# Performance work log

Measured on AMD Instinct MI355X. Metric: run time of the kernel, lower is better.

The kernel has to match this reference:

```python
import jax, jax.numpy as jnp
import numpy as np
from jax import lax

# ---- Haar (db1) wavelet filters, matching create_wavelet_filter ----
_S2 = float(1.0 / np.sqrt(2.0))
_dec_lo = np.array([_S2, _S2], np.float32)    # pywt dec_lo reversed (symmetric)
_dec_hi = np.array([_S2, -_S2], np.float32)   # pywt dec_hi [-s,s] reversed
_rec_lo = np.array([_S2, _S2], np.float32)    # pywt rec_lo flipped (symmetric)
_rec_hi = np.array([-_S2, _S2], np.float32)   # pywt rec_hi [s,-s] flipped

def _outer(a, b):  # torch: a.unsqueeze(0) * b.unsqueeze(1) -> [i,j] = a[j]*b[i]
    return b[:, None] * a[None, :]

DEC = jnp.asarray(np.stack([_outer(_dec_lo, _dec_lo), _outer(_dec_lo, _dec_hi),
                            _outer(_dec_hi, _dec_lo), _outer(_dec_hi, _dec_hi)]))  # [4,2,2]
REC = jnp.asarray(np.stack([_outer(_rec_lo, _rec_lo), _outer(_rec_lo, _rec_hi),
                            _outer(_rec_hi, _rec_lo), _outer(_rec_hi, _rec_hi)]))  # [4,2,2]

BN_EPS = 1e-5

def mish(x):
    return x * jnp.tanh(jax.nn.softplus(x))

def silu(x):
    return x * jax.nn.sigmoid(x)

def bn(x, g, b):  # eval-mode BatchNorm2d with running_mean=0, running_var=1
    return x * (g / jnp.sqrt(1.0 + BN_EPS))[None, :, None, None] + b[None, :, None, None]

def dwconv(x, w, pad):  # depthwise conv, w: [C,1,k,k]
    return lax.conv_general_dilated(x, w, (1, 1), [(pad, pad), (pad, pad)],
                                    feature_group_count=x.shape[1],
                                    dimension_numbers=('NCHW', 'OIHW', 'NCHW'))

def dyn_dwconv(x, ew, gw):
    # DynamicConv2d (depthwise experts). ew: [E,C,1,k,k], gw: [E,C]
    gates = jax.nn.softmax(x.mean((2, 3)) @ gw.T, axis=-1)  # [B,E]
    k = ew.shape[-1]
    outs = jnp.stack([dwconv(x, ew[e], k // 2) for e in range(ew.shape[0])], 1)  # [B,E,C,H,W]
    return jnp.einsum('be,bechw->bchw', gates, outs)

def local_branch(x, ew, gw, bn1g, bn1b, pw, bn2g, bn2b):
    # DWConv2d_BN_ReLU: dynamic dwconv -> BN -> Mish -> depthwise 1x1 (per-channel scale) -> BN
    y = mish(bn(dyn_dwconv(x, ew, gw), bn1g, bn1b))
    y = y * pw[None, :, None, None]
    return bn(y, bn2g, bn2b)

def sel_scan(u, xw, dtw, dtb, Alog, Dp):
    # u: [B,L,D]; xw: [R+2N,D]; dtw: [D,R]; dtb: [D]; Alog: [D,N]; Dp: [D]
    R = dtw.shape[1]
    N = Alog.shape[1]
    xdbl = jnp.einsum('bld,ed->ble', u, xw)
    dt, Bm, Cm = xdbl[..., :R], xdbl[..., R:R + N], xdbl[..., R + N:]
    delta = jax.nn.softplus(jnp.einsum('blr,dr->bld', dt, dtw) + dtb)  # [B,L,D]
    A = -jnp.exp(Alog)                                                  # [D,N]
    a = jnp.exp(delta[..., None] * A)                                   # [B,L,D,N]
    b = delta[..., None] * Bm[:, :, None, :] * u[..., None]             # [B,L,D,N]
    def comb(c1, c2):
        a1, b1 = c1
        a2, b2 = c2
        return a1 * a2, a2 * b1 + b2
    _, h = lax.associative_scan(comb, (a, b), axis=1)                    # h_t = a_t h_{t-1} + b_t
    return jnp.einsum('bldn,bln->bld', h, Cm) + Dp * u

def ss2d(x, in_w, cw, cb, xpw, dtw, dtb, Alog, Dp, ow):
    # SS2D (d_state=1, k_group=2, channel_first): in_proj -> dwconv+silu -> 2-direction
    # selective scan -> gate with silu(z) -> out_proj.
    B, C, H, W = x.shape
    xz = jnp.einsum('oc,bchw->bohw', in_w, x)
    d = in_w.shape[0] // 2
    xi, z = xz[:, :d], xz[:, d:]
    xc = silu(dwconv(xi, cw, 1) + cb[None, :, None, None])
    u0 = xc.reshape(B, d, H * W).transpose(0, 2, 1)                       # row-major scan
    u1 = xc.transpose(0, 1, 3, 2).reshape(B, d, H * W).transpose(0, 2, 1)  # col-major scan
    y0 = sel_scan(u0, xpw[0], dtw[0], dtb[0], Alog[0], Dp[0])
    y1 = sel_scan(u1, xpw[1], dtw[1], dtb[1], Alog[1], Dp[1])
    y0 = y0.transpose(0, 2, 1).reshape(B, d, H, W)
    y1 = y1.transpose(0, 2, 1).reshape(B, d, W, H).transpose(0, 1, 3, 2)
    y = (y0 + y1) * silu(z)
    return jnp.einsum('oc,bchw->bohw', ow, y)

def mbwt(x, wav_w, wav_b, wav_scale, base_scale,
         ss_in_w, ss_conv_w, ss_conv_b, ss_xproj_w, ss_dt_w, ss_dt_b, ss_A_log, ss_D, ss_out_w):
    # MBWTConv2d, wt_levels=1, H/W even. Haar WT (2x2 stride 2) == block reshape + einsum.
    B, C, H, W = x.shape
    xr = x.reshape(B, C, H // 2, 2, W // 2, 2)
    wt = jnp.einsum('bchpwq,kpq->bckhw', xr, DEC)                  # [B,C,4,h,w]
    tag = wt.reshape(B, 4 * C, H // 2, W // 2)
    tag = dwconv(tag, wav_w, wav_w.shape[-1] // 2) + wav_b[None, :, None, None]
    tag = (tag * wav_scale).reshape(B, C, 4, H // 2, W // 2)
    # inverse Haar WT (conv_transpose 2x2 stride 2, groups=C)
    up = jnp.einsum('bckhw,kpq->bchpwq', tag, REC).reshape(B, C, H, W)
    g = ss2d(x, ss_in_w, ss_conv_w, ss_conv_b, ss_xproj_w, ss_dt_w, ss_dt_b, ss_A_log, ss_D, ss_out_w)
    return base_scale * g + up


def setup_inputs() -> dict:
    key = jax.random.key(0)
    ks = iter(jax.random.split(key, 64))
    B, DIM, H, W = 16, 256, 64, 64
    Cg = Cl = 64
    d = {'x': jax.random.normal(next(ks), (B, DIM, H, W), jnp.float32)}
    for j, k in enumerate((3, 5, 7)):
        p = f'l{j}_'
        d[p + 'ew'] = jax.random.normal(next(ks), (4, Cl, 1, k, k), jnp.float32) * 0.1
        d[p + 'gw'] = jax.random.normal(next(ks), (4, Cl), jnp.float32) * 0.1
        d[p + 'bn1g'] = jnp.ones((Cl,), jnp.float32)
        d[p + 'bn1b'] = jnp.zeros((Cl,), jnp.float32)
        d[p + 'pw'] = jax.random.normal(next(ks), (Cl,), jnp.float32) * 0.2
        d[p + 'bn2g'] = jnp.ones((Cl,), jnp.float32)
        d[p + 'bn2b'] = jnp.zeros((Cl,), jnp.float32)
    d['wav_w'] = jax.random.normal(next(ks), (4 * Cg, 1, 3, 3), jnp.float32) * 0.1
    d['wav_b'] = jnp.zeros((4 * Cg,), jnp.float32)
    d['wav_scale'] = jnp.full((1, 4 * Cg, 1, 1), 0.1, jnp.float32)
    d['base_scale'] = jnp.ones((1, Cg, 1, 1), jnp.float32)
    dm, R, N, K = Cg, 4, 1, 2  # d_inner, dt_rank, d_state, k_group
    d['ss_in_w'] = jax.random.normal(next(ks), (2 * dm, Cg), jnp.float32) * float(1 / np.sqrt(Cg))
    d['ss_conv_w'] = jax.random.normal(next(ks), (dm, 1, 3, 3), jnp.float32) * 0.1
    d['ss_conv_b'] = jnp.zeros((dm,), jnp.float32)
    d['ss_xproj_w'] = jax.random.normal(next(ks), (K, R + 2 * N, dm), jnp.float32) * float(1 / np.sqrt(dm))
    d['ss_dt_w'] = jax.random.normal(next(ks), (K, dm, R), jnp.float32) * float(1 / np.sqrt(R))
    d['ss_dt_b'] = jnp.full((K, dm), -2.0, jnp.float32)
    d['ss_A_log'] = jnp.zeros((K, dm, N), jnp.float32)
    d['ss_D'] = jnp.ones((K, dm), jnp.float32)
    d['ss_out_w'] = jax.random.normal(next(ks), (Cg, dm), jnp.float32) * float(1 / np.sqrt(dm))
    return d


def reference(x,
              l0_ew, l0_gw, l0_bn1g, l0_bn1b, l0_pw, l0_bn2g, l0_bn2b,
              l1_ew, l1_gw, l1_bn1g, l1_bn1b, l1_pw, l1_bn2g, l1_bn2b,
              l2_ew, l2_gw, l2_bn1g, l2_bn1b, l2_pw, l2_bn2g, l2_bn2b,
              wav_w, wav_b, wav_scale, base_scale,
              ss_in_w, ss_conv_w, ss_conv_b, ss_xproj_w, ss_dt_w, ss_dt_b, ss_A_log, ss_D, ss_out_w):
    Cg, Cl = 64, 64
    xg, xl, xi = x[:, :Cg], x[:, Cg:Cg + Cl], x[:, Cg + Cl:]
    yl = (local_branch(xl, l0_ew, l0_gw, l0_bn1g, l0_bn1b, l0_pw, l0_bn2g, l0_bn2b)
          + local_branch(xl, l1_ew, l1_gw, l1_bn1g, l1_bn1b, l1_pw, l1_bn2g, l1_bn2b)
          + local_branch(xl, l2_ew, l2_gw, l2_bn1g, l2_bn1b, l2_pw, l2_bn2g, l2_bn2b))
    yg = mbwt(xg, wav_w, wav_b, wav_scale, base_scale,
              ss_in_w, ss_conv_w, ss_conv_b, ss_xproj_w, ss_dt_w, ss_dt_b, ss_A_log, ss_D, ss_out_w)
    return jnp.concatenate([yg, yl, xi], axis=1)
```

## Files before the change

kernel.cpp:

```cpp
#include <hip/hip_runtime.h>
#include <math.h>

static constexpr int NB   = 16;
static constexpr int DIM  = 256;
static constexpr int CG   = 64;
static constexpr int HH   = 64;
static constexpr int WW   = 64;
static constexpr int HW   = HH * WW;

__device__ __forceinline__ float mish_fast(float x) {
    float t = __expf(fminf(x, 20.f));
    float p = __builtin_fmaf(t, t, t + t);
    return x * p * __builtin_amdgcn_rcpf(p + 2.f);
}
__device__ __forceinline__ float silu_f(float x) {
    return x * __builtin_amdgcn_rcpf(1.f + __expf(-x));
}
__device__ __forceinline__ float softplus_fast(float x) {
    return fmaxf(x, 0.f) + __logf(1.f + __expf(-fabsf(x)));
}

__global__ __launch_bounds__(256) void k_stage1(
    const float* __restrict__ x,
    const float* __restrict__ wav_w, const float* __restrict__ wav_b,
    const float* __restrict__ wav_scale,
    float* __restrict__ up, float* __restrict__ mean,
    const float* __restrict__ in_w,
    float* __restrict__ xi, float* __restrict__ z) {
    __shared__ float smem[8192];
    int bid = blockIdx.x;
    int tid = threadIdx.x;

    if (bid % 3 != 2) {
        int aid = (bid / 3) * 2 + (bid % 3);
        int c = aid & 63, b = aid >> 6;
        float* wtb = smem;
        float* red = smem + 4352;
        const float* xp = x + ((size_t)b * DIM + c) * HW;

        {
            const float4* lp4 = (const float4*)(x + ((size_t)b * DIM + 64 + c) * HW);
            float s = 0.f;
            for (int i = tid; i < 1024; i += 256) {
                float4 v = lp4[i];
                s += (v.x + v.y) + (v.z + v.w);
            }
            red[tid] = s;
            __syncthreads();
            for (int o = 128; o > 0; o >>= 1) {
                if (tid < o) red[tid] += red[tid + o];
                __syncthreads();
            }
            if (tid == 0) mean[b * 64 + c] = red[0] * (1.f / HW);
        }

#pragma unroll
        for (int it = 0; it < 2; ++it) {
            int p = tid + it * 256;
            int h = p >> 4, w2 = p & 15;
            float4 top = *(const float4*)(xp + (2 * h) * 64 + 4 * w2);
            float4 bot = *(const float4*)(xp + (2 * h + 1) * 64 + 4 * w2);
            float a0 = top.x, b0 = top.y, c0q = bot.x, d0 = bot.y;
            float a1 = top.z, b1 = top.w, c1q = bot.z, d1 = bot.w;
            int base0 = h * 34 + 2 * w2;
            *(float2*)(wtb + 0 * 1088 + base0) =
                make_float2(0.5f * (a0 + b0 + c0q + d0), 0.5f * (a1 + b1 + c1q + d1));
            *(float2*)(wtb + 1 * 1088 + base0) =
                make_float2(0.5f * (a0 + b0 - c0q - d0), 0.5f * (a1 + b1 - c1q - d1));
            *(float2*)(wtb + 2 * 1088 + base0) =
                make_float2(0.5f * (a0 - b0 + c0q - d0), 0.5f * (a1 - b1 + c1q - d1));
            *(float2*)(wtb + 3 * 1088 + base0) =
                make_float2(0.5f * (a0 - b0 - c0q + d0), 0.5f * (a1 - b1 - c1q + d1));
        }
        __syncthreads();

        float wk[4][9], tb[4];
#pragma unroll
        for (int k = 0; k < 4; ++k) {
            int ch = c * 4 + k;
            float sc = wav_scale[ch];
#pragma unroll
            for (int j = 0; j < 9; ++j) wk[k][j] = wav_w[ch * 9 + j] * sc;
            tb[k] = wav_b[ch] * sc;
        }
        float* upp = up + ((size_t)b * CG + c) * HW;
        for (int i = tid; i < 1024; i += 256) {
            int h = i >> 5, w = i & 31;
            float tg[4];
#pragma unroll
            for (int k = 0; k < 4; ++k) {
                float s = tb[k];
#pragma unroll
                for (int dy = -1; dy <= 1; ++dy) {
                    int hh = h + dy;
                    if (hh < 0 || hh >= 32) continue;
#pragma unroll
                    for (int dx = -1; dx <= 1; ++dx) {
                        int wx = w + dx;
                        if (wx < 0 || wx >= 32) continue;
                        s = fmaf(wtb[k * 1088 + hh * 34 + wx], wk[k][(dy + 1) * 3 + (dx + 1)], s);
                    }
                }
                tg[k] = s;
            }
            float u00 = 0.5f * (tg[0] - tg[1] - tg[2] + tg[3]);
            float u01 = 0.5f * (tg[0] - tg[1] + tg[2] - tg[3]);
            float u10 = 0.5f * (tg[0] + tg[1] - tg[2] - tg[3]);
            float u11 = 0.5f * (tg[0] + tg[1] + tg[2] + tg[3]);
            *(float2*)(upp + (2 * h) * 64 + 2 * w)     = make_float2(u00, u01);
            *(float2*)(upp + (2 * h + 1) * 64 + 2 * w) = make_float2(u10, u11);
        }
    } else {
        int id2 = bid / 3;
        int h0 = (id2 & 31) * 2;
        int b  = id2 >> 5;
        float* xs = smem;
        float* wt = smem + 4096;

        float acc[8][8];
#pragma unroll
        for (int i = 0; i < 8; ++i)
#pragma unroll
            for (int j = 0; j < 8; ++j) acc[i][j] = 0.f;

        int o0 = (tid >> 4) * 8;
        int p0 = (tid & 15) * 8;

        for (int ko = 0; ko < 64; ko += 32) {
            if (ko) __syncthreads();
            {
                int s = tid;
#pragma unroll
                for (int it = 0; it < 4; ++it, s += 256) {
                    int c = s >> 5, p4 = (s & 31) * 4;
                    float4 v = *(const float4*)(x + ((size_t)b * DIM + ko + c) * HW + h0 * 64 + p4);
                    *(float4*)(xs + c * 128 + p4) = v;
                }
            }
            {
                int s = tid;
#pragma unroll
                for (int it = 0; it < 4; ++it, s += 256) {
                    int o = s >> 3, c0 = (s & 7) * 4;
#pragma unroll
                    for (int i = 0; i < 4; ++i) {
                        int cc = c0 + i;
                        int osw = o ^ (((cc >> 2) & 3) << 3);
                        wt[cc * 128 + osw] = ((const float*)(in_w + o * 64 + ko + c0))[i];
                    }
                }
            }
            __syncthreads();
#pragma unroll 4
            for (int c = 0; c < 32; ++c) {
                int osw = o0 ^ (((c >> 2) & 3) << 3);
                float xv[8], wv[8];
                *(float4*)(xv)     = *(const float4*)(xs + c * 128 + p0);
                *(float4*)(xv + 4) = *(const float4*)(xs + c * 128 + p0 + 4);
                *(float4*)(wv)     = *(const float4*)(wt + c * 128 + osw);
                *(float4*)(wv + 4) = *(const float4*)(wt + c * 128 + osw + 4);
#pragma unroll
                for (int i = 0; i < 8; ++i)
#pragma unroll
                    for (int j = 0; j < 8; ++j)
                        acc[i][j] = fmaf(wv[i], xv[j], acc[i][j]);
            }
        }

#pragma unroll
        for (int i = 0; i < 8; ++i) {
            int o = o0 + i;
            float* dst = (o < 64) ? (xi + ((size_t)b * 64 + o) * HW + h0 * 64)
                                  : (z + ((size_t)b * 64 + (o - 64)) * HW + h0 * 64);
            *(float4*)(dst + p0)     = make_float4(acc[i][0], acc[i][1], acc[i][2], acc[i][3]);
            *(float4*)(dst + p0 + 4) = make_float4(acc[i][4], acc[i][5], acc[i][6], acc[i][7]);
        }
    }
}

__global__ __launch_bounds__(256) void k_stage2(
    const float* __restrict__ xi,
    const float* __restrict__ cw, const float* __restrict__ cb,
    const float* __restrict__ xpw,
    float* __restrict__ xc, float4* __restrict__ proj4, float2* __restrict__ projBC,
    const float* __restrict__ mean,
    const float* __restrict__ ew3, const float* __restrict__ gw3, const float* __restrict__ g13,
    const float* __restrict__ ew5, const float* __restrict__ gw5, const float* __restrict__ g15,
    const float* __restrict__ ew7, const float* __restrict__ gw7, const float* __restrict__ g17,
    float* __restrict__ w3o, float* __restrict__ w5o, float* __restrict__ w7o) {
    __shared__ float smem[12608];
    int bid = blockIdx.x;
    int tid = threadIdx.x;

    if (bid < 512) {
        int h0 = (bid & 31) * 2;
        int b  = bid >> 5;
        float* xs  = smem;
        float* xcs = smem + 8448;

        int dir = tid >> 7;
        int px  = tid & 127;
        float acc0 = 0.f, acc1 = 0.f, acc2 = 0.f, acc3 = 0.f, acc4 = 0.f, acc5 = 0.f;

        int cl_c = tid >> 3;
        int p0_c = (tid & 7) * 16;
        int row_c = p0_c >> 6;
        int wb_c  = p0_c & 63;

        for (int ch0 = 0; ch0 < 64; ch0 += 32) {
            if (ch0) __syncthreads();
            {
                int s = tid;
#pragma unroll
                for (int it = 0; it < 8; ++it, s += 256) {
                    int c = s >> 6;
                    int rem = s & 63;
                    int r = rem >> 4, w4 = (rem & 15) * 4;
                    int gh = h0 - 1 + r;
                    float4 v = make_float4(0.f, 0.f, 0.f, 0.f);
                    if (gh >= 0 && gh < 64)
                        v = *(const float4*)(xi + ((size_t)b * 64 + ch0 + c) * HW + gh * 64 + w4);
                    float* dp = xs + c * 264 + r * 66 + 1 + w4;
                    dp[0] = v.x; dp[1] = v.y; dp[2] = v.z; dp[3] = v.w;
                }
                if (tid < 128) {
                    int cl = tid >> 2, r = tid & 3;
                    xs[cl * 264 + r * 66 + 0]  = 0.f;
                    xs[cl * 264 + r * 66 + 65] = 0.f;
                }
            }
            __syncthreads();

            {
                float wk[9];
#pragma unroll
                for (int j = 0; j < 9; ++j) wk[j] = cw[(ch0 + cl_c) * 9 + j];
                float bias = cb[ch0 + cl_c];
                float accr[16];
#pragma unroll
                for (int k = 0; k < 16; ++k) accr[k] = bias;
#pragma unroll
                for (int dy = 0; dy < 3; ++dy) {
                    const float* rp = xs + cl_c * 264 + (row_c + dy) * 66 + wb_c;
                    float r[18];
#pragma unroll
                    for (int q = 0; q < 18; ++q) r[q] = rp[q];
#pragma unroll
                    for (int k = 0; k < 16; ++k)
#pragma unroll
                        for (int dx = 0; dx < 3; ++dx)
                            accr[k] = fmaf(r[k + dx], wk[dy * 3 + dx], accr[k]);
                }
#pragma unroll
                for (int k = 0; k < 16; ++k)
                    xcs[cl_c * 130 + p0_c + k] = silu_f(accr[k]);
            }
            __syncthreads();

            {
                int s = tid;
#pragma unroll
                for (int it = 0; it < 4; ++it, s += 256) {
                    int c = s >> 5, pq = (s & 31) * 4;
                    const float* sp = xcs + c * 130 + pq;
                    *(float4*)(xc + ((size_t)b * 64 + ch0 + c) * HW + h0 * 64 + pq) =
                        make_float4(sp[0], sp[1], sp[2], sp[3]);
                }
            }
            {
                const float* wp = xpw + dir * 6 * 64 + ch0;
#pragma unroll 8
                for (int c = 0; c < 32; ++c) {
                    float xv = xcs[c * 130 + px];
                    acc0 = fmaf(xv, wp[0 * 64 + c], acc0);
                    acc1 = fmaf(xv, wp[1 * 64 + c], acc1);
                    acc2 = fmaf(xv, wp[2 * 64 + c], acc2);
                    acc3 = fmaf(xv, wp[3 * 64 + c], acc3);
                    acc4 = fmaf(xv, wp[4 * 64 + c], acc4);
                    acc5 = fmaf(xv, wp[5 * 64 + c], acc5);
                }
            }
        }

        int h = h0 + (px >> 6), w = px & 63;
        int l = (dir == 0) ? (h * 64 + w) : (w * 64 + h);
        size_t base = ((size_t)dir * NB + b) * HW + l;
        proj4[base]  = make_float4(acc0, acc1, acc2, acc3);
        projBC[base] = make_float2(acc4, acc5);
    } else {
        int b = bid - 512;
        int c = tid;
        float* m = smem;
        float* g = smem + 64;
        if (c < 64) m[c] = mean[b * 64 + c];
        __syncthreads();
        const float rs = rsqrtf(1.f + 1e-5f);

#define WEFF_SECT(GW, EW, G1, OUT, K2)                                        \
        {                                                                     \
            if (c < 4) {                                                      \
                float l = 0.f;                                                \
                for (int cc = 0; cc < 64; ++cc) l += m[cc] * GW[c * 64 + cc]; \
                g[c] = l;                                                     \
            }                                                                 \
            __syncthreads();                                                  \
            if (c == 0) {                                                     \
                float mx = fmaxf(fmaxf(g[0], g[1]), fmaxf(g[2], g[3]));       \
                float e0 = expf(g[0] - mx), e1 = expf(g[1] - mx);             \
                float e2 = expf(g[2] - mx), e3 = expf(g[3] - mx);             \
                float inv = 1.f / (e0 + e1 + e2 + e3);                        \
                g[0] = e0 * inv; g[1] = e1 * inv; g[2] = e2 * inv; g[3] = e3 * inv; \
            }                                                                 \
            __syncthreads();                                                  \
            if (c < 64) {                                                     \
                float g1s = G1[c] * rs;                                       \
                for (int kk = 0; kk < K2; ++kk) {                             \
                    float w = 0.f;                                            \
                    for (int e = 0; e < 4; ++e) w += g[e] * EW[(e * 64 + c) * K2 + kk]; \
                    OUT[(b * 64 + c) * K2 + kk] = w * g1s;                    \
                }                                                             \
            }                                                                 \
            __syncthreads();                                                  \
        }

        WEFF_SECT(gw3, ew3, g13, w3o, 9)
        WEFF_SECT(gw5, ew5, g15, w5o, 25)
        WEFF_SECT(gw7, ew7, g17, w7o, 49)
#undef WEFF_SECT
    }
}

__global__ __launch_bounds__(256) void k_scan2(const float* __restrict__ xc,
                                               const float4* __restrict__ proj4,
                                               const float2* __restrict__ projBC,
                                               const float* __restrict__ dt_w,
                                               const float* __restrict__ dt_b,
                                               const float* __restrict__ A_log,
                                               const float* __restrict__ Dp,
                                               const float* __restrict__ z,
                                               float* __restrict__ yz) {
    int wave = threadIdx.x >> 6;
    int lane = threadIdx.x & 63;
    int wid = blockIdx.x;
    int b = wid >> 6;
    int d = wid & 63;

    __shared__ float ut[64 * 65];
    __shared__ float al[4][1088];
    __shared__ float bl[4][1088];
    __shared__ float aggA[4], aggB[4];

    const float* uplane = xc + ((size_t)b * 64 + d) * HW;
    const float4* up4 = (const float4*)uplane;
#pragma unroll
    for (int q = 0; q < 4; ++q) {
        int s = q * 256 + threadIdx.x;
        float4 v = up4[s];
        int r = s >> 4, c0 = (s & 15) * 4;
        float* p = ut + r * 65 + c0;
        p[0] = v.x; p[1] = v.y; p[2] = v.z; p[3] = v.w;
    }
    __syncthreads();

    int ch = wave;
    float* a_my = al[wave];
    float* b_my = bl[wave];
    float y0r[16];

    {
        float4 wv = *(const float4*)(dt_w + d * 4);
        float db = dt_b[d];
        float A = -__expf(A_log[d]);
        float Dv = Dp[d];
        const float4* p4 = proj4 + (size_t)b * HW;
        const float2* pBC = projBC + (size_t)b * HW;

        float uv[16], cm[16];
#pragma unroll
        for (int j = 0; j < 16; ++j) {
            int el = j * 64 + lane;
            int e  = ch * 1024 + el;
            float4 t4 = p4[e];
            float2 t2 = pBC[e];
            float u = ut[(ch * 16 + j) * 65 + lane];
            uv[j] = u; cm[j] = t2.y;
            float pre = fmaf(t4.x, wv.x, fmaf(t4.y, wv.y,
                        fmaf(t4.z, wv.z, fmaf(t4.w, wv.w, db))));
            float delta = softplus_fast(pre);
            float aj = __expf(delta * A);
            float bj = delta * t2.x * u;
            int idx = (el >> 4) * 17 + (el & 15);
            a_my[idx] = aj;
            b_my[idx] = bj;
        }
        __builtin_amdgcn_wave_barrier();

        float a[16], bb[16];
#pragma unroll
        for (int j = 0; j < 16; ++j) {
            a[j]  = a_my[lane * 17 + j];
            bb[j] = b_my[lane * 17 + j];
        }
        float As = 1.f, Bs = 0.f;
#pragma unroll
        for (int j = 0; j < 16; ++j) { Bs = fmaf(a[j], Bs, bb[j]); As *= a[j]; }
        float Ai = As, Bi = Bs;
#pragma unroll
        for (int off = 1; off < 64; off <<= 1) {
            float ap = __shfl_up(Ai, (unsigned)off, 64);
            float bp = __shfl_up(Bi, (unsigned)off, 64);
            if (lane >= off) { Bi = fmaf(Ai, bp, Bi); Ai *= ap; }
        }
        if (lane == 63) { aggA[wave] = Ai; aggB[wave] = Bi; }
        __syncthreads();
        float carry = 0.f;
        for (int k = 0; k < wave; ++k) carry = fmaf(aggA[k], carry, aggB[k]);
        float ap1 = __shfl_up(Ai, 1, 64);
        float bp1 = __shfl_up(Bi, 1, 64);
        float h = (lane == 0) ? carry : fmaf(ap1, carry, bp1);
#pragma unroll
        for (int j = 0; j < 16; ++j) {
            h = fmaf(a[j], h, bb[j]);
            a_my[lane * 17 + j] = h;
        }
        __builtin_amdgcn_wave_barrier();
#pragma unroll
        for (int j = 0; j < 16; ++j) {
            int el = j * 64 + lane;
            float hv = a_my[(el >> 4) * 17 + (el & 15)];
            y0r[j] = fmaf(hv, cm[j], Dv * uv[j]);
        }
    }
    __syncthreads();

    {
        int pd = 64 + d;
        float4 wv = *(const float4*)(dt_w + pd * 4);
        float db = dt_b[pd];
        float A = -__expf(A_log[pd]);
        float Dv = Dp[pd];
        const float4* p4 = proj4 + ((size_t)NB + b) * HW;
        const float2* pBC = projBC + ((size_t)NB + b) * HW;

        float uv[16], cm[16];
#pragma unroll
        for (int j = 0; j < 16; ++j) {
            int el = j * 64 + lane;
            int e  = ch * 1024 + el;
            float4 t4 = p4[e];
            float2 t2 = pBC[e];
            float u = ut[lane * 65 + (ch * 16 + j)];
            uv[j] = u; cm[j] = t2.y;
            float pre = fmaf(t4.x, wv.x, fmaf(t4.y, wv.y,
                        fmaf(t4.z, wv.z, fmaf(t4.w, wv.w, db))));
            float delta = softplus_fast(pre);
            float aj = __expf(delta * A);
            float bj = delta * t2.x * u;
            int idx = (el >> 4) * 17 + (el & 15);
            a_my[idx] = aj;
            b_my[idx] = bj;
        }
        __builtin_amdgcn_wave_barrier();

        float a[16], bb[16];
#pragma unroll
        for (int j = 0; j < 16; ++j) {
            a[j]  = a_my[lane * 17 + j];
            bb[j] = b_my[lane * 17 + j];
        }
        float As = 1.f, Bs = 0.f;
#pragma unroll
        for (int j = 0; j < 16; ++j) { Bs = fmaf(a[j], Bs, bb[j]); As *= a[j]; }
        float Ai = As, Bi = Bs;
#pragma unroll
        for (int off = 1; off < 64; off <<= 1) {
            float ap = __shfl_up(Ai, (unsigned)off, 64);
            float bp = __shfl_up(Bi, (unsigned)off, 64);
            if (lane >= off) { Bi = fmaf(Ai, bp, Bi); Ai *= ap; }
        }
        if (lane == 63) { aggA[wave] = Ai; aggB[wave] = Bi; }
        __syncthreads();
        float carry = 0.f;
        for (int k = 0; k < wave; ++k) carry = fmaf(aggA[k], carry, aggB[k]);
        float ap1 = __shfl_up(Ai, 1, 64);
        float bp1 = __shfl_up(Bi, 1, 64);
        float h = (lane == 0) ? carry : fmaf(ap1, carry, bp1);
#pragma unroll
        for (int j = 0; j < 16; ++j) {
            h = fmaf(a[j], h, bb[j]);
            a_my[lane * 17 + j] = h;
        }
        __builtin_amdgcn_wave_barrier();
#pragma unroll
        for (int j = 0; j < 16; ++j) {
            int el = j * 64 + lane;
            float hv = a_my[(el >> 4) * 17 + (el & 15)];
            ut[lane * 65 + (ch * 16 + j)] = fmaf(hv, cm[j], Dv * uv[j]);
        }
    }
    __syncthreads();

    const float* zp = z + ((size_t)b * 64 + d) * HW;
    float* yp = yz + ((size_t)b * 64 + d) * HW;
#pragma unroll
    for (int j = 0; j < 16; ++j) {
        int e = ch * 1024 + j * 64 + lane;
        float y1v = ut[(ch * 16 + j) * 65 + lane];
        float zz = zp[e];
        yp[e] = (y0r[j] + y1v) * silu_f(zz);
    }
}

__global__ __launch_bounds__(256) void k_stage4(
    const float* __restrict__ x,
    const float* __restrict__ w3, const float* __restrict__ w5, const float* __restrict__ w7,
    const float* __restrict__ b1_0, const float* __restrict__ pw0,
    const float* __restrict__ g2_0, const float* __restrict__ b2_0,
    const float* __restrict__ b1_1, const float* __restrict__ pw1,
    const float* __restrict__ g2_1, const float* __restrict__ b2_1,
    const float* __restrict__ b1_2, const float* __restrict__ pw2,
    const float* __restrict__ g2_2, const float* __restrict__ b2_2,
    const float* __restrict__ yz, const float* __restrict__ ow,
    const float* __restrict__ base_scale, const float* __restrict__ up,
    float* __restrict__ out) {
    __shared__ float smem[6144];
    int bid = blockIdx.x;
    int tid = threadIdx.x;

    if (bid % 9 != 8) {
        int cidx = (bid / 9) * 8 + (bid % 9);
        int tile = cidx & 3;
        int c = (cidx >> 2) & 63;
        int b = cidx >> 8;
        int oy = (tile >> 1) * 32, ox = (tile & 1) * 32;
        float* t = smem;
        const float* xp = x + ((size_t)b * DIM + 64 + c) * HW;
        for (int i = tid; i < 38 * 38; i += 256) {
            int r = i / 38, cc = i % 38;
            int yy = r - 3 + oy, xx = cc - 3 + ox;
            t[r * 40 + cc] = (yy >= 0 && yy < 64 && xx >= 0 && xx < 64) ? xp[yy * 64 + xx] : 0.f;
        }
        {
            const float4* x4 = (const float4*)x;
            float4* o4 = (float4*)out;
            int base = cidx * 512;
#pragma unroll
            for (int it = 0; it < 2; ++it) {
                int idx = base + it * 256 + tid;
                int bb = idx >> 17;
                int r  = idx & 131071;
                int gi = bb * 262144 + 131072 + r;
                o4[gi] = x4[gi];
            }
        }
        const float* w3p = w3 + (b * 64 + c) * 9;
        const float* w5p = w5 + (b * 64 + c) * 25;
        const float* w7p = w7 + (b * 64 + c) * 49;
        float W3r[9], W5r[25], W7r[49];
#pragma unroll
        for (int j = 0; j < 9; ++j)  W3r[j] = w3p[j];
#pragma unroll
        for (int j = 0; j < 25; ++j) W5r[j] = w5p[j];
#pragma unroll
        for (int j = 0; j < 49; ++j) W7r[j] = w7p[j];
        __syncthreads();

        const float rs = rsqrtf(1.f + 1e-5f);
        float bb1a = b1_0[c], bb1b = b1_1[c], bb1c = b1_2[c];
        float ssa = pw0[c] * g2_0[c] * rs, ssb = pw1[c] * g2_1[c] * rs, ssc = pw2[c] * g2_2[c] * rs;
        float bb2a = b2_0[c], bb2b = b2_1[c], bb2c = b2_2[c];

        int y  = tid >> 3;
        int x0 = (tid & 7) * 4;

        float a3[4] = {0.f, 0.f, 0.f, 0.f};
        float a5[4] = {0.f, 0.f, 0.f, 0.f};
        float a7[4] = {0.f, 0.f, 0.f, 0.f};

#pragma unroll
        for (int dy = 0; dy < 7; ++dy) {
            const float4* rp = (const float4*)(t + (y + dy) * 40 + x0);
            float4 q0 = rp[0], q1 = rp[1], q2 = rp[2];
            float r[12] = {q0.x, q0.y, q0.z, q0.w, q1.x, q1.y, q1.z, q1.w,
                           q2.x, q2.y, q2.z, q2.w};
#pragma unroll
            for (int k = 0; k < 4; ++k)
#pragma unroll
                for (int dx = 0; dx < 7; ++dx)
                    a7[k] = fmaf(r[k + dx], W7r[dy * 7 + dx], a7[k]);
            if (dy >= 1 && dy <= 5) {
                int ey = dy - 1;
#pragma unroll
                for (int k = 0; k < 4; ++k)
#pragma unroll
                    for (int dx = 0; dx < 5; ++dx)
                        a5[k] = fmaf(r[k + 1 + dx], W5r[ey * 5 + dx], a5[k]);
            }
            if (dy >= 2 && dy <= 4) {
                int ey = dy - 2;
#pragma unroll
                for (int k = 0; k < 4; ++k)
#pragma unroll
                    for (int dx = 0; dx < 3; ++dx)
                        a3[k] = fmaf(r[k + 2 + dx], W3r[ey * 3 + dx], a3[k]);
            }
        }

        float4 res;
        float* rr = (float*)&res;
#pragma unroll
        for (int k = 0; k < 4; ++k) {
            rr[k] = mish_fast(a3[k] + bb1a) * ssa + bb2a
                  + mish_fast(a5[k] + bb1b) * ssb + bb2b
                  + mish_fast(a7[k] + bb1c) * ssc + bb2c;
        }
        float* op = out + ((size_t)b * DIM + 64 + c) * HW;
        *(float4*)(op + (oy + y) * 64 + ox + x0) = res;
    } else {
        int id2 = bid / 9;
        int h0 = (id2 & 31) * 2;
        int b  = id2 >> 5;
        float* yv = smem;
        float* wt = smem + 4096;

        float acc[8][4];
#pragma unroll
        for (int i = 0; i < 8; ++i)
#pragma unroll
            for (int j = 0; j < 4; ++j) acc[i][j] = 0.f;

        int o0 = (tid >> 5) * 8;
        int p0 = (tid & 31) * 4;

        for (int ko = 0; ko < 64; ko += 32) {
            if (ko) __syncthreads();
            {
                int s = tid;
#pragma unroll
                for (int it = 0; it < 4; ++it, s += 256) {
                    int c = s >> 5, p4 = (s & 31) * 4;
                    size_t idx = ((size_t)b * 64 + ko + c) * HW + h0 * 64 + p4;
                    *(float4*)(yv + c * 128 + p4) = *(const float4*)(yz + idx);
                }
            }
            {
                int s = tid;
#pragma unroll
                for (int it = 0; it < 2; ++it, s += 256) {
                    int o = s >> 3, c0 = (s & 7) * 4;
#pragma unroll
                    for (int i = 0; i < 4; ++i) {
                        int cc = c0 + i;
                        int osw = o ^ (((cc >> 2) & 3) << 3);
                        wt[cc * 64 + osw] = ((const float*)(ow + o * 64 + ko + c0))[i];
                    }
                }
            }
            __syncthreads();
#pragma unroll 4
            for (int c = 0; c < 32; ++c) {
                int osw = o0 ^ (((c >> 2) & 3) << 3);
                float wv[8], xv[4];
                *(float4*)(wv)     = *(const float4*)(wt + c * 64 + osw);
                *(float4*)(wv + 4) = *(const float4*)(wt + c * 64 + osw + 4);
                *(float4*)(xv)     = *(const float4*)(yv + c * 128 + p0);
#pragma unroll
                for (int i = 0; i < 8; ++i)
#pragma unroll
                    for (int j = 0; j < 4; ++j)
                        acc[i][j] = fmaf(wv[i], xv[j], acc[i][j]);
            }
        }

#pragma unroll
        for (int i = 0; i < 8; ++i) {
            int o = o0 + i;
            float bs = base_scale[o];
            float4 u = *(const float4*)(up + ((size_t)b * 64 + o) * HW + h0 * 64 + p0);
            float4 r = make_float4(fmaf(bs, acc[i][0], u.x),
                                   fmaf(bs, acc[i][1], u.y),
                                   fmaf(bs, acc[i][2], u.z),
                                   fmaf(bs, acc[i][3], u.w));
            *(float4*)(out + ((size_t)b * DIM + o) * HW + h0 * 64 + p0) = r;
        }
    }
}

extern "C" void kernel_launch(void* const* d_in, const int* in_sizes, int n_in,
                              void* d_out, int out_size, void* d_ws, size_t ws_size,
                              hipStream_t stream) {
    (void)in_sizes; (void)n_in; (void)out_size; (void)ws_size;
    const float* x = (const float*)d_in[0];
    float* out = (float*)d_out;
    float* ws = (float*)d_ws;

    const size_t IMG = (size_t)NB * 64 * HW;
    float* buf_xi   = ws;
    float* buf_z    = ws + IMG;
    float* buf_xc   = ws + 2 * IMG;
    float* buf_up   = ws + 3 * IMG;
    float* buf_p4   = ws + 4 * IMG;
    float* buf_pBC  = buf_p4 + (size_t)4 * 2 * NB * HW;
    float* buf_mean = buf_pBC + (size_t)2 * 2 * NB * HW;
    float* buf_w3   = buf_mean + 1024;
    float* buf_w5   = buf_w3 + 16 * 64 * 9;
    float* buf_w7   = buf_w5 + 16 * 64 * 25;

    k_stage1<<<1536, 256, 0, stream>>>(x,
        (const float*)d_in[22], (const float*)d_in[23], (const float*)d_in[24],
        buf_up, buf_mean,
        (const float*)d_in[26], buf_xi, buf_z);

    k_stage2<<<528, 256, 0, stream>>>(buf_xi,
        (const float*)d_in[27], (const float*)d_in[28], (const float*)d_in[29],
        buf_xc, (float4*)buf_p4, (float2*)buf_pBC,
        buf_mean,
        (const float*)d_in[1],  (const float*)d_in[2],  (const float*)d_in[3],
        (const float*)d_in[8],  (const float*)d_in[9],  (const float*)d_in[10],
        (const float*)d_in[15], (const float*)d_in[16], (const float*)d_in[17],
        buf_w3, buf_w5, buf_w7);

    k_scan2<<<1024, 256, 0, stream>>>(buf_xc, (const float4*)buf_p4, (const float2*)buf_pBC,
        (const float*)d_in[30], (const float*)d_in[31],
        (const float*)d_in[32], (const float*)d_in[33],
        buf_z, buf_xi);

    k_stage4<<<4608, 256, 0, stream>>>(x, buf_w3, buf_w5, buf_w7,
        (const float*)d_in[4],  (const float*)d_in[5],  (const float*)d_in[6],  (const float*)d_in[7],
        (const float*)d_in[11], (const float*)d_in[12], (const float*)d_in[13], (const float*)d_in[14],
        (const float*)d_in[18], (const float*)d_in[19], (const float*)d_in[20], (const float*)d_in[21],
        buf_xi, (const float*)d_in[34], (const float*)d_in[25], buf_up, out);
}
```

Before: 117.7 us.

## Halve shared-memory tiles and move passthrough copy into stage1 spare blocks

Shrinks the channel chunk of the GEMM-like loops in stage1, stage2 and stage4 from 32 to 16, halving their shared memory so more blocks can be resident per CU. Moves the identity passthrough copy of the last 128 channels from stage4 into a new block role in stage1, and rebalances the stage1 block-role interleave to 4:2:1. Weight loads are now vectorised as float4. The cost is more loop iterations and more __syncthreads per block.

```diff
diff --git a/kernel.cpp b/kernel.cpp
--- a/kernel.cpp
+++ b/kernel.cpp
@@ -26,13 +26,15 @@
     const float* __restrict__ wav_scale,
     float* __restrict__ up, float* __restrict__ mean,
     const float* __restrict__ in_w,
-    float* __restrict__ xi, float* __restrict__ z) {
-    __shared__ float smem[8192];
+    float* __restrict__ xi, float* __restrict__ z,
+    float* __restrict__ out) {
+    __shared__ float smem[4608];
     int bid = blockIdx.x;
     int tid = threadIdx.x;
-
-    if (bid % 3 != 2) {
-        int aid = (bid / 3) * 2 + (bid % 3);
+    int role = bid % 7;
+
+    if (role < 4) {
+        int aid = (bid / 7) * 4 + role;
         int c = aid & 63, b = aid >> 6;
         float* wtb = smem;
         float* red = smem + 4352;
@@ -110,12 +112,12 @@
             *(float2*)(upp + (2 * h) * 64 + 2 * w)     = make_float2(u00, u01);
             *(float2*)(upp + (2 * h + 1) * 64 + 2 * w) = make_float2(u10, u11);
         }
-    } else {
-        int id2 = bid / 3;
-        int h0 = (id2 & 31) * 2;
-        int b  = id2 >> 5;
+    } else if (role < 6) {
+        int did = (bid / 7) * 2 + (role - 4);
+        int h0 = (did & 31) * 2;
+        int b  = did >> 5;
         float* xs = smem;
-        float* wt = smem + 4096;
+        float* wt = smem + 2048;
 
         float acc[8][8];
 #pragma unroll
@@ -126,12 +128,12 @@
         int o0 = (tid >> 4) * 8;
         int p0 = (tid & 15) * 8;
 
-        for (int ko = 0; ko < 64; ko += 32) {
+        for (int ko = 0; ko < 64; ko += 16) {
             if (ko) __syncthreads();
             {
                 int s = tid;
 #pragma unroll
-                for (int it = 0; it < 4; ++it, s += 256) {
+                for (int it = 0; it < 2; ++it, s += 256) {
                     int c = s >> 5, p4 = (s & 31) * 4;
                     float4 v = *(const float4*)(x + ((size_t)b * DIM + ko + c) * HW + h0 * 64 + p4);
                     *(float4*)(xs + c * 128 + p4) = v;
@@ -140,19 +142,20 @@
             {
                 int s = tid;
 #pragma unroll
-                for (int it = 0; it < 4; ++it, s += 256) {
-                    int o = s >> 3, c0 = (s & 7) * 4;
+                for (int it = 0; it < 2; ++it, s += 256) {
+                    int o = s >> 2, c0 = (s & 3) * 4;
+                    float4 v = *(const float4*)(in_w + o * 64 + ko + c0);
 #pragma unroll
                     for (int i = 0; i < 4; ++i) {
                         int cc = c0 + i;
                         int osw = o ^ (((cc >> 2) & 3) << 3);
-                        wt[cc * 128 + osw] = ((const float*)(in_w + o * 64 + ko + c0))[i];
+                        wt[cc * 128 + osw] = ((const float*)&v)[i];
                     }
                 }
             }
             __syncthreads();
 #pragma unroll 4
-            for (int c = 0; c < 32; ++c) {
+            for (int c = 0; c < 16; ++c) {
                 int osw = o0 ^ (((c >> 2) & 3) << 3);
                 float xv[8], wv[8];
                 *(float4*)(xv)     = *(const float4*)(xs + c * 128 + p0);
@@ -174,6 +177,19 @@
                                   : (z + ((size_t)b * 64 + (o - 64)) * HW + h0 * 64);
             *(float4*)(dst + p0)     = make_float4(acc[i][0], acc[i][1], acc[i][2], acc[i][3]);
             *(float4*)(dst + p0 + 4) = make_float4(acc[i][4], acc[i][5], acc[i][6], acc[i][7]);
+        }
+    } else {
+        int pid = bid / 7;
+        const float4* x4 = (const float4*)x;
+        float4* o4 = (float4*)out;
+        int base = pid * 8192;
+#pragma unroll
+        for (int it = 0; it < 32; ++it) {
+            int idx = base + it * 256 + tid;
+            int bb = idx >> 17;
+            int r  = idx & 131071;
+            int gi = bb * 262144 + 131072 + r;
+            o4[gi] = x4[gi];
         }
     }
 }
@@ -188,7 +204,7 @@
     const float* __restrict__ ew5, const float* __restrict__ gw5, const float* __restrict__ g15,
     const float* __restrict__ ew7, const float* __restrict__ gw7, const float* __restrict__ g17,
     float* __restrict__ w3o, float* __restrict__ w5o, float* __restrict__ w7o) {
-    __shared__ float smem[12608];
+    __shared__ float smem[6304];
     int bid = blockIdx.x;
     int tid = threadIdx.x;
 
@@ -196,23 +212,23 @@
         int h0 = (bid & 31) * 2;
         int b  = bid >> 5;
         float* xs  = smem;
-        float* xcs = smem + 8448;
+        float* xcs = smem + 4224;
 
         int dir = tid >> 7;
         int px  = tid & 127;
         float acc0 = 0.f, acc1 = 0.f, acc2 = 0.f, acc3 = 0.f, acc4 = 0.f, acc5 = 0.f;
 
-        int cl_c = tid >> 3;
-        int p0_c = (tid & 7) * 16;
+        int cl_c = tid >> 4;
+        int p0_c = (tid & 15) * 8;
         int row_c = p0_c >> 6;
         int wb_c  = p0_c & 63;
 
-        for (int ch0 = 0; ch0 < 64; ch0 += 32) {
+        for (int ch0 = 0; ch0 < 64; ch0 += 16) {
             if (ch0) __syncthreads();
             {
                 int s = tid;
 #pragma unroll
-                for (int it = 0; it < 8; ++it, s += 256) {
+                for (int it = 0; it < 4; ++it, s += 256) {
                     int c = s >> 6;
                     int rem = s & 63;
                     int r = rem >> 4, w4 = (rem & 15) * 4;
@@ -223,7 +239,7 @@
                     float* dp = xs + c * 264 + r * 66 + 1 + w4;
                     dp[0] = v.x; dp[1] = v.y; dp[2] = v.z; dp[3] = v.w;
                 }
-                if (tid < 128) {
+                if (tid < 64) {
                     int cl = tid >> 2, r = tid & 3;
                     xs[cl * 264 + r * 66 + 0]  = 0.f;
                     xs[cl * 264 + r * 66 + 65] = 0.f;
@@ -236,23 +252,23 @@
 #pragma unroll
                 for (int j = 0; j < 9; ++j) wk[j] = cw[(ch0 + cl_c) * 9 + j];
                 float bias = cb[ch0 + cl_c];
-                float accr[16];
-#pragma unroll
-                for (int k = 0; k < 16; ++k) accr[k] = bias;
+                float accr[8];
+#pragma unroll
+                for (int k = 0; k < 8; ++k) accr[k] = bias;
 #pragma unroll
                 for (int dy = 0; dy < 3; ++dy) {
                     const float* rp = xs + cl_c * 264 + (row_c + dy) * 66 + wb_c;
-                    float r[18];
-#pragma unroll
-                    for (int q = 0; q < 18; ++q) r[q] = rp[q];
-#pragma unroll
-                    for (int k = 0; k < 16; ++k)
+                    float r[10];
+#pragma unroll
+                    for (int q = 0; q < 10; ++q) r[q] = rp[q];
+#pragma unroll
+                    for (int k = 0; k < 8; ++k)
 #pragma unroll
                         for (int dx = 0; dx < 3; ++dx)
                             accr[k] = fmaf(r[k + dx], wk[dy * 3 + dx], accr[k]);
                 }
 #pragma unroll
-                for (int k = 0; k < 16; ++k)
+                for (int k = 0; k < 8; ++k)
                     xcs[cl_c * 130 + p0_c + k] = silu_f(accr[k]);
             }
             __syncthreads();
@@ -260,7 +276,7 @@
             {
                 int s = tid;
 #pragma unroll
-                for (int it = 0; it < 4; ++it, s += 256) {
+                for (int it = 0; it < 2; ++it, s += 256) {
                     int c = s >> 5, pq = (s & 31) * 4;
                     const float* sp = xcs + c * 130 + pq;
                     *(float4*)(xc + ((size_t)b * 64 + ch0 + c) * HW + h0 * 64 + pq) =
@@ -270,7 +286,7 @@
             {
                 const float* wp = xpw + dir * 6 * 64 + ch0;
 #pragma unroll 8
-                for (int c = 0; c < 32; ++c) {
+                for (int c = 0; c < 16; ++c) {
                     float xv = xcs[c * 130 + px];
                     acc0 = fmaf(xv, wp[0 * 64 + c], acc0);
                     acc1 = fmaf(xv, wp[1 * 64 + c], acc1);
@@ -523,7 +539,7 @@
     const float* __restrict__ yz, const float* __restrict__ ow,
     const float* __restrict__ base_scale, const float* __restrict__ up,
     float* __restrict__ out) {
-    __shared__ float smem[6144];
+    __shared__ float smem[3072];
     int bid = blockIdx.x;
     int tid = threadIdx.x;
 
@@ -540,19 +556,6 @@
             int yy = r - 3 + oy, xx = cc - 3 + ox;
             t[r * 40 + cc] = (yy >= 0 && yy < 64 && xx >= 0 && xx < 64) ? xp[yy * 64 + xx] : 0.f;
         }
-        {
-            const float4* x4 = (const float4*)x;
-            float4* o4 = (float4*)out;
-            int base = cidx * 512;
-#pragma unroll
-            for (int it = 0; it < 2; ++it) {
-                int idx = base + it * 256 + tid;
-                int bb = idx >> 17;
-                int r  = idx & 131071;
-                int gi = bb * 262144 + 131072 + r;
-                o4[gi] = x4[gi];
-            }
-        }
         const float* w3p = w3 + (b * 64 + c) * 9;
         const float* w5p = w5 + (b * 64 + c) * 25;
         const float* w7p = w7 + (b * 64 + c) * 49;
@@ -621,7 +624,7 @@
         int h0 = (id2 & 31) * 2;
         int b  = id2 >> 5;
         float* yv = smem;
-        float* wt = smem + 4096;
+        float* wt = smem + 2048;
 
         float acc[8][4];
 #pragma unroll
@@ -632,33 +635,30 @@
         int o0 = (tid >> 5) * 8;
         int p0 = (tid & 31) * 4;
 
-        for (int ko = 0; ko < 64; ko += 32) {
+        for (int ko = 0; ko < 64; ko += 16) {
             if (ko) __syncthreads();
             {
                 int s = tid;
 #pragma unroll
-                for (int it = 0; it < 4; ++it, s += 256) {
+                for (int it = 0; it < 2; ++it, s += 256) {
                     int c = s >> 5, p4 = (s & 31) * 4;
                     size_t idx = ((size_t)b * 64 + ko + c) * HW + h0 * 64 + p4;
                     *(float4*)(yv + c * 128 + p4) = *(const float4*)(yz + idx);
                 }
             }
             {
-                int s = tid;
-#pragma unroll
-                for (int it = 0; it < 2; ++it, s += 256) {
-                    int o = s >> 3, c0 = (s & 7) * 4;
-#pragma unroll
-                    for (int i = 0; i < 4; ++i) {
-                        int cc = c0 + i;
-                        int osw = o ^ (((cc >> 2) & 3) << 3);
-                        wt[cc * 64 + osw] = ((const float*)(ow + o * 64 + ko + c0))[i];
-                    }
+                int o = tid >> 2, c0 = (tid & 3) * 4;
+                float4 v = *(const float4*)(ow + o * 64 + ko + c0);
+#pragma unroll
+                for (int i = 0; i < 4; ++i) {
+                    int cc = c0 + i;
+                    int osw = o ^ (((cc >> 2) & 3) << 3);
+                    wt[cc * 64 + osw] = ((const float*)&v)[i];
                 }
             }
             __syncthreads();
 #pragma unroll 4
-            for (int c = 0; c < 32; ++c) {
+            for (int c = 0; c < 16; ++c) {
                 int osw = o0 ^ (((c >> 2) & 3) << 3);
                 float wv[8], xv[4];
                 *(float4*)(wv)     = *(const float4*)(wt + c * 64 + osw);
@@ -706,10 +706,10 @@
     float* buf_w5   = buf_w3 + 16 * 64 * 9;
     float* buf_w7   = buf_w5 + 16 * 64 * 25;
 
-    k_stage1<<<1536, 256, 0, stream>>>(x,
+    k_stage1<<<1792, 256, 0, stream>>>(x,
         (const float*)d_in[22], (const float*)d_in[23], (const float*)d_in[24],
         buf_up, buf_mean,
-        (const float*)d_in[26], buf_xi, buf_z);
+        (const float*)d_in[26], buf_xi, buf_z, out);
 
     k_stage2<<<528, 256, 0, stream>>>(buf_xi,
         (const float*)d_in[27], (const float*)d_in[28], (const float*)d_in[29],
```

Result: slower. 120.2 us (+2.1%).
